# Optimization experiments

Hardware: AMD Instinct MI355X
Metric: run time of the kernel (lower is better)

The kernel has to match this reference:

```python
import jax, jax.numpy as jnp
import numpy as np

B, S, H, NH = 4, 1024, 1024, 16
DH = H // NH
EPS = 1e-12  # BERT layer_norm_eps


def layer_norm(x, scale, bias, eps=EPS):
    mu = jnp.mean(x, axis=-1, keepdims=True)
    var = jnp.var(x, axis=-1, keepdims=True)
    return (x - mu) / jnp.sqrt(var + eps) * scale + bias


def setup_inputs() -> dict:
    key = jax.random.key(0)
    ks = jax.random.split(key, 8)
    lin = lambda k: jax.random.normal(k, (H, H), jnp.float32) * 0.02
    zeros_h = jnp.zeros((H,), jnp.float32)
    return {
        "hidden_states": jax.random.normal(ks[0], (B, S, H), jnp.float32),
        "group_prob": jnp.zeros((B, S, S), jnp.float32),
        "attention_mask": jnp.ones((B, 1, S, S), jnp.int32),
        "Wq": lin(ks[1]), "bq": zeros_h,
        "Wk": lin(ks[2]), "bk": zeros_h,
        "Wv": lin(ks[3]), "bv": zeros_h,
        "gWq": lin(ks[4]), "gbq": zeros_h,
        "gWk": lin(ks[5]), "gbk": zeros_h,
        "g_ln_scale": jnp.ones((H,), jnp.float32), "g_ln_bias": zeros_h,
        "Wo": lin(ks[6]), "bo": zeros_h,
        "out_ln_scale": jnp.ones((H,), jnp.float32), "out_ln_bias": zeros_h,
    }


def _forward(hidden_states, group_prob, attention_mask, Wq, bq, Wk, bk, Wv, bv,
             gWq, gbq, gWk, gbk, g_ln_scale, g_ln_bias, Wo, bo,
             out_ln_scale, out_ln_bias):
    am = attention_mask.astype(jnp.int32)              # [B,1,S,S]
    a = jnp.eye(S, k=1, dtype=jnp.int32)               # superdiagonal
    b = jnp.eye(S, dtype=jnp.int32)                    # identity
    c = jnp.eye(S, k=-1, dtype=jnp.int32)              # subdiagonal
    tri = jnp.triu(jnp.ones((S, S), jnp.float32))      # upper tri incl diag

    # ---- GroupAttention (tree-transformer constituent priors) ----
    hs = layer_norm(hidden_states, g_ln_scale, g_ln_bias)
    gq = hs @ gWq.T + gbq
    gk = hs @ gWk.T + gbk
    g_scores = jnp.einsum('bqd,bkd->bqk', gq, gk) / jnp.float32(H)
    g_mask = (am & (a + c))[:, 0]                      # [B,S,S] tridiag band, no diag
    g_scores = jnp.where(g_mask == 0, -jnp.inf, g_scores)
    n_attn = jnp.nan_to_num(jax.nn.softmax(g_scores, axis=-1))
    n_attn = jnp.sqrt(n_attn * jnp.swapaxes(n_attn, -1, -2) + 1e-9)
    n_attn = group_prob + (1.0 - group_prob) * n_attn  # prior mixing
    t = jnp.where(a == 0, 0.0, jnp.log(n_attn + 1e-9)) @ tri
    g_attn = jnp.exp(tri @ t)
    strict_upper = tri.astype(jnp.int32) - b           # nonzero on strict upper tri
    g_attn = jnp.where(strict_upper == 0, 0.0, g_attn)
    g_attn = g_attn + jnp.swapaxes(g_attn, -1, -2) + jnp.where(b == 0, 1e-9, n_attn)
    break_prob = n_attn

    # ---- BertSelfAttention, mode 'L' ----
    def split_heads(x):
        return x.reshape(B, S, NH, DH).transpose(0, 2, 1, 3)  # [B,NH,S,DH]
    q = split_heads(hidden_states @ Wq.T + bq)
    k = split_heads(hidden_states @ Wk.T + bk)
    v = split_heads(hidden_states @ Wv.T + bv)
    scores = jnp.einsum('bhqd,bhkd->bhqk', q, k) / jnp.sqrt(jnp.float32(DH))
    keep = (am | b) != 0                               # diag always attended
    scores = jnp.where(keep, scores, -jnp.inf)
    probs = jax.nn.softmax(scores, axis=-1)
    probs = probs * g_attn[:, None]                    # group-prob reweighting
    ctx = jnp.einsum('bhqk,bhkd->bhqd', probs, v)
    ctx = ctx.transpose(0, 2, 1, 3).reshape(B, S, H)

    # ---- BertSelfOutput: dense + residual + LayerNorm ----
    out = layer_norm(ctx @ Wo.T + bo + hidden_states, out_ln_scale, out_ln_bias)
    return out, scores, g_attn, break_prob


def reference(hidden_states, group_prob, attention_mask, Wq, bq, Wk, bk, Wv, bv,
              gWq, gbq, gWk, gbk, g_ln_scale, g_ln_bias, Wo, bo,
              out_ln_scale, out_ln_bias):
    return _forward(hidden_states, group_prob, attention_mask, Wq, bq, Wk, bk,
                    Wv, bv, gWq, gbq, gWk, gbk, g_ln_scale, g_ln_bias, Wo, bo,
                    out_ln_scale, out_ln_bias)
```

## Files before the change

kernel.cpp:

```cpp
#include <hip/hip_runtime.h>
#include <math.h>

#define BB 4
#define S 1024
#define H 1024
#define NHD 16
#define DH 64
#define LN_EPS 1e-12f
#define SQ9 3.1622776601683795e-5f
#define NEG_INF (-__builtin_inff())
#define L2E 1.4426950408889634f

typedef unsigned short u16;
typedef unsigned int u32;
using bfrag = __attribute__((ext_vector_type(8))) short;
using f32x4 = __attribute__((ext_vector_type(4))) float;

typedef __attribute__((address_space(1))) void void_g;
typedef __attribute__((address_space(3))) void void_l;

__device__ __forceinline__ void gload16(const void* g, void* l) {
  __builtin_amdgcn_global_load_lds((void_g*)g, (void_l*)l, 16, 0, 0);
}

__device__ __forceinline__ u16 f2bf(float f) {
  u32 u = __builtin_bit_cast(u32, f);
  u32 r = (u + 0x7fffu + ((u >> 16) & 1u)) >> 16;
  return (u16)r;
}
__device__ __forceinline__ float bf2f(u32 b) {
  u32 u = b << 16;
  return __builtin_bit_cast(float, u);
}

__device__ __forceinline__ float sum16_dpp(float x) {
  int v;
  v = __builtin_amdgcn_mov_dpp(__builtin_bit_cast(int, x), 0xB1, 0xF, 0xF, true);
  x += __builtin_bit_cast(float, v);
  v = __builtin_amdgcn_mov_dpp(__builtin_bit_cast(int, x), 0x4E, 0xF, 0xF, true);
  x += __builtin_bit_cast(float, v);
  v = __builtin_amdgcn_mov_dpp(__builtin_bit_cast(int, x), 0x124, 0xF, 0xF, true);
  x += __builtin_bit_cast(float, v);
  v = __builtin_amdgcn_mov_dpp(__builtin_bit_cast(int, x), 0x128, 0xF, 0xF, true);
  x += __builtin_bit_cast(float, v);
  return x;
}

__device__ __forceinline__ float block_sum256(float v, float* buf) {
#pragma unroll
  for (int o = 32; o > 0; o >>= 1) v += __shfl_down(v, o);
  if ((threadIdx.x & 63) == 0) buf[threadIdx.x >> 6] = v;
  __syncthreads();
  float r = buf[0] + buf[1] + buf[2] + buf[3];
  __syncthreads();
  return r;
}

__global__ __launch_bounds__(256) void prep_kernel(
    const float* __restrict__ Wq, const float* __restrict__ Wk, const float* __restrict__ Wv,
    const float* __restrict__ gWq, const float* __restrict__ gWk,
    const float* __restrict__ hidden, const int* __restrict__ am,
    const float* __restrict__ glns, const float* __restrict__ glnb,
    u16* __restrict__ dstW, u32* __restrict__ amb, u16* __restrict__ hsbf) {
  __shared__ float buf[4];
  int bid = blockIdx.x;
  if (bid < 9216) {
    const int WQ = 262144;
    int i = bid * 256 + threadIdx.x;
    const float* src; int off;
    if      (i < 1 * WQ) { src = Wq;  off = 0; }
    else if (i < 2 * WQ) { src = Wk;  off = 1 * WQ; }
    else if (i < 3 * WQ) { src = Wv;  off = 2 * WQ; }
    else if (i < 4 * WQ) { src = gWq; off = 3 * WQ; }
    else if (i < 5 * WQ) { src = gWk; off = 4 * WQ; }
    else                 { src = hidden; off = 5 * WQ; }
    float4 v = reinterpret_cast<const float4*>(src)[i - off];
    u32 lo = (u32)f2bf(v.x) | ((u32)f2bf(v.y) << 16);
    u32 hi = (u32)f2bf(v.z) | ((u32)f2bf(v.w) << 16);
    reinterpret_cast<uint2*>(dstW)[i] = make_uint2(lo, hi);
  } else if (bid < 25600) {
    size_t t = (size_t)(bid - 9216) * 256 + threadIdx.x;
    int v = am[t] != 0;
    unsigned long long m = __ballot(v);
    int lane = threadIdx.x & 63;
    if (lane == 0)       amb[t >> 5] = (u32)m;
    else if (lane == 32) amb[t >> 5] = (u32)(m >> 32);
  } else {
    size_t row = bid - 25600;
    const float4 xv = reinterpret_cast<const float4*>(hidden + row * H)[threadIdx.x];
    float s  = xv.x + xv.y + xv.z + xv.w;
    float s2 = xv.x * xv.x + xv.y * xv.y + xv.z * xv.z + xv.w * xv.w;
    s  = block_sum256(s, buf);
    s2 = block_sum256(s2, buf);
    float mu  = s * (1.0f / H);
    float var = s2 * (1.0f / H) - mu * mu;
    float inv = rsqrtf(var + LN_EPS);
    const float4 sv = reinterpret_cast<const float4*>(glns)[threadIdx.x];
    const float4 bv = reinterpret_cast<const float4*>(glnb)[threadIdx.x];
    float o0 = (xv.x - mu) * inv * sv.x + bv.x;
    float o1 = (xv.y - mu) * inv * sv.y + bv.y;
    float o2 = (xv.z - mu) * inv * sv.z + bv.z;
    float o3 = (xv.w - mu) * inv * sv.w + bv.w;
    u32 lo = (u32)f2bf(o0) | ((u32)f2bf(o1) << 16);
    u32 hi = (u32)f2bf(o2) | ((u32)f2bf(o3) << 16);
    reinterpret_cast<uint2*>(hsbf + row * H)[threadIdx.x] = make_uint2(lo, hi);
  }
}

__global__ __launch_bounds__(256) void mega_gemm(
    const u16* __restrict__ hbf, const u16* __restrict__ hsbf,
    const u16* __restrict__ Wcat,
    const float* __restrict__ bq, const float* __restrict__ bk, const float* __restrict__ bv,
    const float* __restrict__ gbq, const float* __restrict__ gbk,
    u16* __restrict__ q, u16* __restrict__ k, u16* __restrict__ vt,
    u16* __restrict__ gq, u16* __restrict__ gk) {
  __shared__ __align__(16) u16 SM[32768];
  const int Kdim = H;
  int fid = blockIdx.x + blockIdx.y * 40;
  int swz = (fid & 7) * 160 + (fid >> 3);
  int lx = swz % 40, ly = swz / 40;
  int which = lx >> 3;
  const u16* A = (which < 3) ? hbf : hsbf;
  int rowBlk = ly * 128, colBlk = lx * 128;
  int tid = threadIdx.x, wid = tid >> 6, l = tid & 63;
  int dr = l >> 3, sl = l & 7;
  int co = (sl ^ dr) << 3;
  const u16* Ag = A + (size_t)rowBlk * Kdim;
  const u16* Bg = Wcat + (size_t)colBlk * Kdim;
  f32x4 acc[4][4];
#pragma unroll
  for (int i = 0; i < 4; ++i)
#pragma unroll
    for (int j = 0; j < 4; ++j) acc[i][j] = (f32x4){0.f, 0.f, 0.f, 0.f};
#pragma unroll
  for (int i = 0; i < 4; ++i) {
    int L = wid * 4 + i;
    gload16(Ag + (size_t)(L * 8 + dr) * Kdim + co, &SM[L * 512]);
    gload16(Bg + (size_t)(L * 8 + dr) * Kdim + co, &SM[16384 + L * 512]);
  }
  __syncthreads();
  int wm = wid >> 1, wn = wid & 1;
  const int nt = Kdim >> 6;
  int buf = 0;
  int sw = (l & 7) << 4;
  for (int t = 0; t < nt; ++t) {
    if (t + 1 < nt) {
      int k0 = (t + 1) << 6;
      int dstoff = (buf ^ 1) * 8192;
#pragma unroll
      for (int i = 0; i < 4; ++i) {
        int L = wid * 4 + i;
        gload16(Ag + (size_t)(L * 8 + dr) * Kdim + k0 + co, &SM[dstoff + L * 512]);
        gload16(Bg + (size_t)(L * 8 + dr) * Kdim + k0 + co, &SM[16384 + dstoff + L * 512]);
      }
    }
    const char* Ab = (const char*)&SM[buf * 8192];
    const char* Bb = (const char*)&SM[16384 + buf * 8192];
#pragma unroll
    for (int ks = 0; ks < 2; ++ks) {
      int kb = (ks * 64 + ((l >> 4) << 4)) ^ sw;
      bfrag af[4], bfv[4];
#pragma unroll
      for (int mi = 0; mi < 4; ++mi)
        af[mi] = *(const bfrag*)(Ab + (wm * 64 + mi * 16 + (l & 15)) * 128 + kb);
#pragma unroll
      for (int ni = 0; ni < 4; ++ni)
        bfv[ni] = *(const bfrag*)(Bb + (wn * 64 + ni * 16 + (l & 15)) * 128 + kb);
#pragma unroll
      for (int mi = 0; mi < 4; ++mi)
#pragma unroll
        for (int ni = 0; ni < 4; ++ni)
          acc[mi][ni] = __builtin_amdgcn_mfma_f32_16x16x32_bf16(af[mi], bfv[ni], acc[mi][ni], 0, 0, 0);
    }
    __syncthreads();
    buf ^= 1;
  }
  const float* bias = (which == 0) ? bq : (which == 1) ? bk : (which == 2) ? bv
                      : (which == 3) ? gbq : gbk;
  if (which == 2) {
    u16* T = SM;
#pragma unroll
    for (int mi = 0; mi < 4; ++mi) {
#pragma unroll
      for (int ni = 0; ni < 4; ++ni) {
        int c = wn * 64 + ni * 16 + (l & 15);
        float bvv = bias[(colBlk & 1023) + c];
        int tokb = wm * 64 + mi * 16 + ((l >> 4) << 2);
        u32 w0 = (u32)f2bf(acc[mi][ni][0] + bvv) | ((u32)f2bf(acc[mi][ni][1] + bvv) << 16);
        u32 w1 = (u32)f2bf(acc[mi][ni][2] + bvv) | ((u32)f2bf(acc[mi][ni][3] + bvv) << 16);
        *(u32*)&T[c * 144 + tokb]     = w0;
        *(u32*)&T[c * 144 + tokb + 2] = w1;
      }
    }
    __syncthreads();
    int col = tid >> 1, th = tid & 1;
    int g = (colBlk & 1023) + col;
    int bb = rowBlk >> 10;
    int s0 = (rowBlk & 1023) + th * 64;
    const uint4* src = (const uint4*)&T[col * 144 + th * 64];
    u16* dst = vt + ((size_t)(bb * 1024 + g)) * S + s0;
#pragma unroll
    for (int i = 0; i < 8; ++i) reinterpret_cast<uint4*>(dst)[i] = src[i];
  } else {
    u16* O = (which == 0) ? q : (which == 1) ? k : (which == 3) ? gq : gk;
#pragma unroll
    for (int mi = 0; mi < 4; ++mi) {
#pragma unroll
      for (int ni = 0; ni < 4; ++ni) {
        int col = (colBlk + wn * 64 + ni * 16 + (l & 15)) & 1023;
        float bvv = bias[col];
#pragma unroll
        for (int j = 0; j < 4; ++j) {
          int row = rowBlk + wm * 64 + mi * 16 + ((l >> 4) << 2) + j;
          O[(size_t)row * H + col] = f2bf(acc[mi][ni][j] + bvv);
        }
      }
    }
  }
}

__global__ __launch_bounds__(256) void gemm_dense(
    const u16* __restrict__ A, const u16* __restrict__ Bw,
    const float* __restrict__ bias, const float* __restrict__ resid,
    u16* __restrict__ C) {
  __shared__ __align__(16) u16 SM[32768];
  const int Kdim = H;
  int fid = blockIdx.x + blockIdx.y * 8;
  int swz = (fid & 7) * 32 + (fid >> 3);
  int lx = swz & 7, ly = swz >> 3;
  int rowBlk = ly * 128, colBlk = lx * 128;
  int tid = threadIdx.x, wid = tid >> 6, l = tid & 63;
  int dr = l >> 3, sl = l & 7;
  int co = (sl ^ dr) << 3;
  const u16* Ag = A + (size_t)rowBlk * Kdim;
  const u16* Bg = Bw + (size_t)colBlk * Kdim;
  f32x4 acc[4][4];
#pragma unroll
  for (int i = 0; i < 4; ++i)
#pragma unroll
    for (int j = 0; j < 4; ++j) acc[i][j] = (f32x4){0.f, 0.f, 0.f, 0.f};
#pragma unroll
  for (int i = 0; i < 4; ++i) {
    int L = wid * 4 + i;
    gload16(Ag + (size_t)(L * 8 + dr) * Kdim + co, &SM[L * 512]);
    gload16(Bg + (size_t)(L * 8 + dr) * Kdim + co, &SM[16384 + L * 512]);
  }
  __syncthreads();
  int wm = wid >> 1, wn = wid & 1;
  const int nt = Kdim >> 6;
  int buf = 0;
  int sw = (l & 7) << 4;
  for (int t = 0; t < nt; ++t) {
    if (t + 1 < nt) {
      int k0 = (t + 1) << 6;
      int dstoff = (buf ^ 1) * 8192;
#pragma unroll
      for (int i = 0; i < 4; ++i) {
        int L = wid * 4 + i;
        gload16(Ag + (size_t)(L * 8 + dr) * Kdim + k0 + co, &SM[dstoff + L * 512]);
        gload16(Bg + (size_t)(L * 8 + dr) * Kdim + k0 + co, &SM[16384 + dstoff + L * 512]);
      }
    }
    const char* Ab = (const char*)&SM[buf * 8192];
    const char* Bb = (const char*)&SM[16384 + buf * 8192];
#pragma unroll
    for (int ks = 0; ks < 2; ++ks) {
      int kb = (ks * 64 + ((l >> 4) << 4)) ^ sw;
      bfrag af[4], bfv[4];
#pragma unroll
      for (int mi = 0; mi < 4; ++mi)
        af[mi] = *(const bfrag*)(Ab + (wm * 64 + mi * 16 + (l & 15)) * 128 + kb);
#pragma unroll
      for (int ni = 0; ni < 4; ++ni)
        bfv[ni] = *(const bfrag*)(Bb + (wn * 64 + ni * 16 + (l & 15)) * 128 + kb);
#pragma unroll
      for (int mi = 0; mi < 4; ++mi)
#pragma unroll
        for (int ni = 0; ni < 4; ++ni)
          acc[mi][ni] = __builtin_amdgcn_mfma_f32_16x16x32_bf16(af[mi], bfv[ni], acc[mi][ni], 0, 0, 0);
    }
    __syncthreads();
    buf ^= 1;
  }
#pragma unroll
  for (int mi = 0; mi < 4; ++mi) {
#pragma unroll
    for (int ni = 0; ni < 4; ++ni) {
      int col = colBlk + wn * 64 + ni * 16 + (l & 15);
      float bvv = bias[col];
#pragma unroll
      for (int j = 0; j < 4; ++j) {
        int row = rowBlk + wm * 64 + mi * 16 + ((l >> 4) << 2) + j;
        C[(size_t)row * H + col] = f2bf(acc[mi][ni][j] + bvv + resid[(size_t)row * H + col]);
      }
    }
  }
}

__global__ __launch_bounds__(256) void band_dots_kernel(
    const u16* __restrict__ gq, const u16* __restrict__ gk,
    const float* __restrict__ Wo, u16* __restrict__ Wobf,
    float* __restrict__ znext, float* __restrict__ zprev) {
  __shared__ float buf[4];
  int bid = blockIdx.x;
  if (bid >= 4096) {
    int i = (bid - 4096) * 256 + threadIdx.x;
    float4 v = reinterpret_cast<const float4*>(Wo)[i];
    u32 lo = (u32)f2bf(v.x) | ((u32)f2bf(v.y) << 16);
    u32 hi = (u32)f2bf(v.z) | ((u32)f2bf(v.w) << 16);
    reinterpret_cast<uint2*>(Wobf)[i] = make_uint2(lo, hi);
    return;
  }
  size_t idx = bid;
  int i = (int)(idx & (S - 1));
  uint2 q2 = reinterpret_cast<const uint2*>(gq + idx * H)[threadIdx.x];
  float q0 = bf2f(q2.x & 0xffff), q1 = bf2f(q2.x >> 16);
  float q2f = bf2f(q2.y & 0xffff), q3 = bf2f(q2.y >> 16);
  float dn = 0.f, dp = 0.f;
  if (i < S - 1) {
    uint2 k2 = reinterpret_cast<const uint2*>(gk + (idx + 1) * H)[threadIdx.x];
    dn = q0 * bf2f(k2.x & 0xffff) + q1 * bf2f(k2.x >> 16) +
         q2f * bf2f(k2.y & 0xffff) + q3 * bf2f(k2.y >> 16);
  }
  if (i > 0) {
    uint2 k2 = reinterpret_cast<const uint2*>(gk + (idx - 1) * H)[threadIdx.x];
    dp = q0 * bf2f(k2.x & 0xffff) + q1 * bf2f(k2.x >> 16) +
         q2f * bf2f(k2.y & 0xffff) + q3 * bf2f(k2.y >> 16);
  }
  dn = block_sum256(dn, buf);
  dp = block_sum256(dp, buf);
  if (threadIdx.x == 0) { znext[idx] = dn; zprev[idx] = dp; }
}

__global__ __launch_bounds__(1024) void band_prefix_kernel(
    const float* __restrict__ znext, const float* __restrict__ zprev,
    const int* __restrict__ am, const float* __restrict__ gp,
    float* __restrict__ sband, float* __restrict__ Cpre) {
  __shared__ float pd[S];
  __shared__ float scn[S];
  int b = blockIdx.x, i = threadIdx.x;
  size_t idx = (size_t)b * S + i;
  bool luv = (i < S - 1) && (am[((size_t)b * S + i) * S + i + 1] != 0);
  bool ldv = (i > 0) && (am[((size_t)b * S + i) * S + i - 1] != 0);
  float pf, pdn;
  if (!luv && !ldv) { pf = 0.f; pdn = 0.f; }
  else if (!ldv)    { pf = 1.f; pdn = 0.f; }
  else if (!luv)    { pf = 0.f; pdn = 1.f; }
  else {
    float lu = znext[idx] * (1.0f / (float)H);
    float ld = zprev[idx] * (1.0f / (float)H);
    float m = fmaxf(lu, ld);
    float eu = expf(lu - m), ed = expf(ld - m);
    float inv = 1.f / (eu + ed);
    pf = eu * inv; pdn = ed * inv;
  }
  pd[i] = pdn;
  __syncthreads();
  float sb = 0.f, L = 0.f;
  if (i < S - 1) {
    sb = sqrtf(pf * pd[i + 1] + 1e-9f);
    float gpv = gp[((size_t)b * S + i) * S + (i + 1)];
    float nm = gpv + (1.f - gpv) * sb;
    L = logf(nm + 1e-9f);
  }
  sband[idx] = sb;
  scn[i] = L;
  __syncthreads();
  for (int off = 1; off < S; off <<= 1) {
    float t = (i >= off) ? scn[i - off] : 0.f;
    __syncthreads();
    scn[i] += t;
    __syncthreads();
  }
  Cpre[idx] = (i > 0) ? scn[i - 1] : 0.f;
}

__global__ __launch_bounds__(256) void gattn_write_kernel(
    const float* __restrict__ gp, const float* __restrict__ sband,
    const float* __restrict__ Cpre, float* __restrict__ ga, float* __restrict__ brk) {
  __shared__ float Crow[S];
  __shared__ float Srow[S];
  size_t bi = blockIdx.x;
  int b = (int)(bi >> 10), i = (int)(bi & (S - 1));
  reinterpret_cast<float4*>(Crow)[threadIdx.x] =
      reinterpret_cast<const float4*>(Cpre + (size_t)b * S)[threadIdx.x];
  reinterpret_cast<float4*>(Srow)[threadIdx.x] =
      reinterpret_cast<const float4*>(sband + (size_t)b * S)[threadIdx.x];
  __syncthreads();
  float Ci = Crow[i];
  size_t rowoff = bi * S;
  const float4 g4 = reinterpret_cast<const float4*>(gp + rowoff)[threadIdx.x];
  const float gparr[4] = {g4.x, g4.y, g4.z, g4.w};
  float go[4], bo_[4];
#pragma unroll
  for (int j = 0; j < 4; ++j) {
    int k = threadIdx.x * 4 + j;
    float gpv = gparr[j];
    float gav;
    if (k == i) {
      gav = gpv + (1.f - gpv) * SQ9;
    } else {
      float d = (k > i) ? (Crow[k] - Ci) : (Ci - Crow[k]);
      gav = expf(d) + 1e-9f;
    }
    float sval = (k == i + 1) ? Srow[i] : ((k == i - 1) ? Srow[k] : SQ9);
    go[j]  = gav;
    bo_[j] = gpv + (1.f - gpv) * sval;
  }
  f32x4 go4 = (f32x4){go[0], go[1], go[2], go[3]};
  __builtin_nontemporal_store(go4, reinterpret_cast<f32x4*>(ga + rowoff) + threadIdx.x);
  f32x4 bo4 = (f32x4){bo_[0], bo_[1], bo_[2], bo_[3]};
  __builtin_nontemporal_store(bo4, reinterpret_cast<f32x4*>(brk + rowoff) + threadIdx.x);
}

__global__ __launch_bounds__(512) void flash_kernel(
    const u16* __restrict__ q, const u16* __restrict__ k, const u16* __restrict__ vt,
    const u32* __restrict__ amb, const float* __restrict__ Cpre,
    const float* __restrict__ gp,
    float* __restrict__ scores, u16* __restrict__ ctx) {
  __shared__ __align__(16) u16 QPt[8192];
  __shared__ __align__(16) u16 Kt[2][4096];
  __shared__ __align__(16) u16 Vt[2][4096];
  __shared__ float CLds[1024];
  int fid = blockIdx.x + blockIdx.y * 8;
  int qb = (fid >> 3) & 7;
  int bh = (fid & 7) * 8 + (fid >> 6);
  int b = bh >> 4, h = bh & 15;
  int tid = threadIdx.x, wid = tid >> 6, l = tid & 63;
  int dr = l >> 3, sl = l & 7;
  int co = (sl ^ dr) << 3;
  const u16* qbase = q + ((size_t)b * S + qb * 128) * H + h * 64;
  const u16* kbase = k + (size_t)b * S * H + h * 64;
  const u16* vtb   = vt + (size_t)bh * 64 * S;
  {
    float2 c2 = reinterpret_cast<const float2*>(Cpre + (size_t)b * S)[tid];
    c2.x *= L2E; c2.y *= L2E;
    reinterpret_cast<float2*>(CLds)[tid] = c2;
  }
#pragma unroll
  for (int i = 0; i < 2; ++i) {
    int L = wid * 2 + i;
    gload16(qbase + (size_t)(L * 8 + dr) * H + co, &QPt[L * 512]);
  }
  gload16(kbase + (size_t)(wid * 8 + dr) * H + co, &Kt[0][wid * 512]);
  gload16(vtb + (size_t)(wid * 8 + dr) * S + co, &Vt[0][wid * 512]);
  __syncthreads();
  int sw = (l & 7) << 4;
  int qr = l & 15;
  bfrag qa[2];
#pragma unroll
  for (int ks = 0; ks < 2; ++ks) {
    int kb = (ks * 64 + ((l >> 4) << 4)) ^ sw;
    qa[ks] = *(const bfrag*)((const char*)QPt + (wid * 16 + qr) * 128 + kb);
  }
  __syncthreads();
  int rowg0 = qb * 128 + wid * 16 + ((l >> 4) << 2);
  float Ci2[4], gdiag[4];
#pragma unroll
  for (int j = 0; j < 4; ++j) {
    int row = rowg0 + j;
    Ci2[j] = CLds[row];
    float gpd = gp[((size_t)b * S + row) * S + row];
    gdiag[j] = gpd + (1.f - gpd) * SQ9;
  }
  float l_loc[4];
  f32x4 oacc[4];
#pragma unroll
  for (int j = 0; j < 4; ++j) l_loc[j] = 0.f;
#pragma unroll
  for (int nb = 0; nb < 4; ++nb) oacc[nb] = (f32x4){0.f, 0.f, 0.f, 0.f};
  uint2 wcur[4];
#pragma unroll
  for (int j = 0; j < 4; ++j)
    wcur[j] = *reinterpret_cast<const uint2*>(amb + ((size_t)b * S + rowg0 + j) * 32);
  int cur = 0;
  for (int kt = 0; kt < 16; ++kt) {
    uint2 wnxt[4];
    if (kt < 15) {
      gload16(kbase + (size_t)((kt + 1) * 64 + wid * 8 + dr) * H + co, &Kt[cur ^ 1][wid * 512]);
      gload16(vtb + (size_t)(wid * 8 + dr) * S + (kt + 1) * 64 + co, &Vt[cur ^ 1][wid * 512]);
#pragma unroll
      for (int j = 0; j < 4; ++j)
        wnxt[j] = *reinterpret_cast<const uint2*>(
            amb + ((size_t)b * S + rowg0 + j) * 32 + (kt + 1) * 2);
    }
    f32x4 acc[4];
#pragma unroll
    for (int nb = 0; nb < 4; ++nb) acc[nb] = (f32x4){0.f, 0.f, 0.f, 0.f};
    __builtin_amdgcn_s_setprio(1);
#pragma unroll
    for (int ks = 0; ks < 2; ++ks) {
      int kb = (ks * 64 + ((l >> 4) << 4)) ^ sw;
#pragma unroll
      for (int nb = 0; nb < 4; ++nb) {
        bfrag bv = *(const bfrag*)((const char*)Kt[cur] + (nb * 16 + qr) * 128 + kb);
        acc[nb] = __builtin_amdgcn_mfma_f32_16x16x32_bf16(qa[ks], bv, acc[nb], 0, 0, 0);
      }
    }
    __builtin_amdgcn_s_setprio(0);
    float vals[4][4];
#pragma unroll
    for (int j = 0; j < 4; ++j) {
      int row = rowg0 + j;
      float* srow = scores + ((size_t)bh * S + row) * S + kt * 64;
#pragma unroll
      for (int nb = 0; nb < 4; ++nb) {
        int col = nb * 16 + qr;
        int colg = kt * 64 + col;
        u32 word = (nb < 2) ? wcur[j].x : wcur[j].y;
        int keep = (int)((word >> (col & 31)) & 1u) | (row == colg);
        float v = keep ? acc[nb][j] * 0.125f : NEG_INF;
        vals[nb][j] = v;
        __builtin_nontemporal_store(v, srow + col);
      }
    }
    float Ck2[4];
#pragma unroll
    for (int nb = 0; nb < 4; ++nb) Ck2[nb] = CLds[kt * 64 + nb * 16 + qr];
#pragma unroll
    for (int j = 0; j < 4; ++j) {
      int row = rowg0 + j;
      int prow = wid * 16 + ((l >> 4) << 2) + j;
      char* ptrow = (char*)QPt + prow * 128;
      int psw = (prow & 7) << 4;
      float pp[4], pg[4];
#pragma unroll
      for (int nb = 0; nb < 4; ++nb) {
        float t = vals[nb][j] * L2E;
        pp[nb] = exp2f(t);
        int colg = kt * 64 + nb * 16 + qr;
        float d2 = (colg > row) ? (Ck2[nb] - Ci2[j]) : (Ci2[j] - Ck2[nb]);
        float g = exp2f(t + d2);
        pg[nb] = (colg == row) ? pp[nb] * gdiag[j] : g;
      }
      l_loc[j] += pp[0] + pp[1] + pp[2] + pp[3];
#pragma unroll
      for (int nb = 0; nb < 4; ++nb)
        *(u16*)(ptrow + (((nb * 16 + qr) * 2) ^ psw)) = f2bf(pg[nb]);
    }
    __builtin_amdgcn_s_setprio(1);
#pragma unroll
    for (int ks = 0; ks < 2; ++ks) {
      int kb = (ks * 64 + ((l >> 4) << 4)) ^ sw;
      bfrag pa = *(const bfrag*)((const char*)QPt + (wid * 16 + qr) * 128 + kb);
#pragma unroll
      for (int nb = 0; nb < 4; ++nb) {
        bfrag vv = *(const bfrag*)((const char*)Vt[cur] + (nb * 16 + qr) * 128 + kb);
        oacc[nb] = __builtin_amdgcn_mfma_f32_16x16x32_bf16(pa, vv, oacc[nb], 0, 0, 0);
      }
    }
    __builtin_amdgcn_s_setprio(0);
    asm volatile("s_waitcnt vmcnt(16)" ::: "memory");
    __builtin_amdgcn_s_barrier();
    __builtin_amdgcn_sched_barrier(0);
    if (kt < 15) {
#pragma unroll
      for (int j = 0; j < 4; ++j) wcur[j] = wnxt[j];
    }
    cur ^= 1;
  }
#pragma unroll
  for (int j = 0; j < 4; ++j) l_loc[j] = sum16_dpp(l_loc[j]);
#pragma unroll
  for (int j = 0; j < 4; ++j) {
    int row = rowg0 + j;
    float ir = 1.f / l_loc[j];
#pragma unroll
    for (int nb = 0; nb < 4; ++nb) {
      int d = nb * 16 + qr;
      ctx[((size_t)b * S + row) * H + h * 64 + d] = f2bf(oacc[nb][j] * ir);
    }
  }
}

__global__ __launch_bounds__(256) void ln_bf_kernel(
    const u16* __restrict__ x, const float* __restrict__ sc,
    const float* __restrict__ bi, float* __restrict__ y) {
  __shared__ float buf[4];
  size_t row = blockIdx.x;
  uint2 xv = reinterpret_cast<const uint2*>(x + row * H)[threadIdx.x];
  float x0 = bf2f(xv.x & 0xffff), x1 = bf2f(xv.x >> 16);
  float x2 = bf2f(xv.y & 0xffff), x3 = bf2f(xv.y >> 16);
  float s  = x0 + x1 + x2 + x3;
  float s2 = x0 * x0 + x1 * x1 + x2 * x2 + x3 * x3;
  s  = block_sum256(s, buf);
  s2 = block_sum256(s2, buf);
  float mu  = s * (1.0f / H);
  float var = s2 * (1.0f / H) - mu * mu;
  float inv = rsqrtf(var + LN_EPS);
  const float4 sv = reinterpret_cast<const float4*>(sc)[threadIdx.x];
  const float4 bv = reinterpret_cast<const float4*>(bi)[threadIdx.x];
  float4 o;
  o.x = (x0 - mu) * inv * sv.x + bv.x;
  o.y = (x1 - mu) * inv * sv.y + bv.y;
  o.z = (x2 - mu) * inv * sv.z + bv.z;
  o.w = (x3 - mu) * inv * sv.w + bv.w;
  reinterpret_cast<float4*>(y + row * H)[threadIdx.x] = o;
}

extern "C" void kernel_launch(void* const* d_in, const int* in_sizes, int n_in,
                              void* d_out, int out_size, void* d_ws, size_t ws_size,
                              hipStream_t stream) {
  const float* hidden = (const float*)d_in[0];
  const float* gp     = (const float*)d_in[1];
  const int*   am     = (const int*)d_in[2];
  const float* Wq = (const float*)d_in[3];  const float* bq = (const float*)d_in[4];
  const float* Wk = (const float*)d_in[5];  const float* bk = (const float*)d_in[6];
  const float* Wv = (const float*)d_in[7];  const float* bv = (const float*)d_in[8];
  const float* gWq = (const float*)d_in[9]; const float* gbq = (const float*)d_in[10];
  const float* gWk = (const float*)d_in[11];const float* gbk = (const float*)d_in[12];
  const float* glns = (const float*)d_in[13]; const float* glnb = (const float*)d_in[14];
  const float* Wo = (const float*)d_in[15]; const float* bo = (const float*)d_in[16];
  const float* olns = (const float*)d_in[17]; const float* olnb = (const float*)d_in[18];

  float* out    = (float*)d_out;
  float* scores = out + (size_t)BB * S * H;
  float* gattn  = scores + (size_t)BB * NHD * S * S;
  float* brk    = gattn + (size_t)BB * S * S;

  const size_t MB = 1u << 20;
  char* w = (char*)d_ws;
  u16* Wcat  = (u16*)(w);
  u16* hbf   = (u16*)(w + 10 * MB);
  u16* ctxbf = hbf;
  u16* hsbf  = (u16*)(w + 18 * MB);
  u16* Wobf  = hsbf;
  u16* qbf   = (u16*)(w + 26 * MB);
  u16* kbf   = (u16*)(w + 34 * MB);
  u16* vtb   = (u16*)(w + 42 * MB);
  u16* gqbf  = (u16*)(w + 50 * MB);
  u16* densebf = gqbf;
  u16* gkbf  = (u16*)(w + 58 * MB);
  u32* amb   = (u32*)(w + 66 * MB);
  float* znext  = (float*)(w + 66 * MB + 512 * 1024);
  float* zprev  = znext + BB * S;
  float* sbandA = zprev + BB * S;
  float* CpreA  = sbandA + BB * S;

  dim3 blk(256);

  prep_kernel<<<29696, blk, 0, stream>>>(Wq, Wk, Wv, gWq, gWk, hidden, am,
                                         glns, glnb, Wcat, amb, hsbf);

  mega_gemm<<<dim3(40, 32), blk, 0, stream>>>(hbf, hsbf, Wcat,
                                              bq, bk, bv, gbq, gbk,
                                              qbf, kbf, vtb, gqbf, gkbf);

  band_dots_kernel<<<5120, blk, 0, stream>>>(gqbf, gkbf, Wo, Wobf, znext, zprev);
  band_prefix_kernel<<<BB, 1024, 0, stream>>>(znext, zprev, am, gp, sbandA, CpreA);
  gattn_write_kernel<<<BB * S, blk, 0, stream>>>(gp, sbandA, CpreA, gattn, brk);

  flash_kernel<<<dim3(8, 64), dim3(512), 0, stream>>>(qbf, kbf, vtb, amb, CpreA,
                                                      gp, scores, ctxbf);

  gemm_dense<<<dim3(8, 32), blk, 0, stream>>>(ctxbf, Wobf, bo, hidden, densebf);
  ln_bf_kernel<<<BB * S, blk, 0, stream>>>(densebf, olns, olnb, out);
}
```

Before: 230.1 us.

## Transpose QK^T MFMA so each lane owns a row, vectorize score and P stores

Swaps the MFMA operand order for S = QK^T so the accumulator holds a transposed tile, giving each lane one query row and four consecutive key columns. This lets the scores output be written as 16-byte nontemporal vector stores instead of scalar stores, lets the bf16 P tile be written to LDS as packed 64-bit stores, and reduces per-lane mask and diagonal state to a single row. The row-sum for normalization now needs a cross-lane shuffle plus an LDS exchange and barrier, because the output accumulator layout still maps rows differently from the score layout.

```diff
diff --git a/kernel.cpp b/kernel.cpp
--- a/kernel.cpp
+++ b/kernel.cpp
@@ -13,6 +13,7 @@
 
 typedef unsigned short u16;
 typedef unsigned int u32;
+typedef unsigned long long u64;
 using bfrag = __attribute__((ext_vector_type(8))) short;
 using f32x4 = __attribute__((ext_vector_type(4))) float;
 
@@ -31,19 +32,6 @@
 __device__ __forceinline__ float bf2f(u32 b) {
   u32 u = b << 16;
   return __builtin_bit_cast(float, u);
-}
-
-__device__ __forceinline__ float sum16_dpp(float x) {
-  int v;
-  v = __builtin_amdgcn_mov_dpp(__builtin_bit_cast(int, x), 0xB1, 0xF, 0xF, true);
-  x += __builtin_bit_cast(float, v);
-  v = __builtin_amdgcn_mov_dpp(__builtin_bit_cast(int, x), 0x4E, 0xF, 0xF, true);
-  x += __builtin_bit_cast(float, v);
-  v = __builtin_amdgcn_mov_dpp(__builtin_bit_cast(int, x), 0x124, 0xF, 0xF, true);
-  x += __builtin_bit_cast(float, v);
-  v = __builtin_amdgcn_mov_dpp(__builtin_bit_cast(int, x), 0x128, 0xF, 0xF, true);
-  x += __builtin_bit_cast(float, v);
-  return x;
 }
 
 __device__ __forceinline__ float block_sum256(float v, float* buf) {
@@ -422,11 +410,13 @@
   __shared__ __align__(16) u16 Kt[2][4096];
   __shared__ __align__(16) u16 Vt[2][4096];
   __shared__ float CLds[1024];
+  __shared__ float Lsc[128];
   int fid = blockIdx.x + blockIdx.y * 8;
   int qb = (fid >> 3) & 7;
   int bh = (fid & 7) * 8 + (fid >> 6);
   int b = bh >> 4, h = bh & 15;
   int tid = threadIdx.x, wid = tid >> 6, l = tid & 63;
+  int hi = l >> 4, qr = l & 15;
   int dr = l >> 3, sl = l & 7;
   int co = (sl ^ dr) << 3;
   const u16* qbase = q + ((size_t)b * S + qb * 128) * H + h * 64;
@@ -446,43 +436,33 @@
   gload16(vtb + (size_t)(wid * 8 + dr) * S + co, &Vt[0][wid * 512]);
   __syncthreads();
   int sw = (l & 7) << 4;
-  int qr = l & 15;
   bfrag qa[2];
 #pragma unroll
   for (int ks = 0; ks < 2; ++ks) {
-    int kb = (ks * 64 + ((l >> 4) << 4)) ^ sw;
+    int kb = (ks * 64 + (hi << 4)) ^ sw;
     qa[ks] = *(const bfrag*)((const char*)QPt + (wid * 16 + qr) * 128 + kb);
   }
   __syncthreads();
-  int rowg0 = qb * 128 + wid * 16 + ((l >> 4) << 2);
-  float Ci2[4], gdiag[4];
-#pragma unroll
-  for (int j = 0; j < 4; ++j) {
-    int row = rowg0 + j;
-    Ci2[j] = CLds[row];
-    float gpd = gp[((size_t)b * S + row) * S + row];
-    gdiag[j] = gpd + (1.f - gpd) * SQ9;
-  }
-  float l_loc[4];
+  int myrow = qb * 128 + wid * 16 + qr;
+  float Ci2 = CLds[myrow];
+  float gpd = gp[((size_t)b * S + myrow) * S + myrow];
+  float gdiagS = gpd + (1.f - gpd) * SQ9;
+  float* srowbase = scores + ((size_t)bh * S + myrow) * S;
+  char* ptrow = (char*)QPt + (wid * 16 + qr) * 128;
+  int psw = (qr & 7) << 4;
+  float l_loc = 0.f;
   f32x4 oacc[4];
 #pragma unroll
-  for (int j = 0; j < 4; ++j) l_loc[j] = 0.f;
-#pragma unroll
   for (int nb = 0; nb < 4; ++nb) oacc[nb] = (f32x4){0.f, 0.f, 0.f, 0.f};
-  uint2 wcur[4];
-#pragma unroll
-  for (int j = 0; j < 4; ++j)
-    wcur[j] = *reinterpret_cast<const uint2*>(amb + ((size_t)b * S + rowg0 + j) * 32);
+  uint2 wcur = *reinterpret_cast<const uint2*>(amb + (size_t)myrow * 32 + (size_t)b * S * 32);
   int cur = 0;
   for (int kt = 0; kt < 16; ++kt) {
-    uint2 wnxt[4];
+    uint2 wnxt;
     if (kt < 15) {
       gload16(kbase + (size_t)((kt + 1) * 64 + wid * 8 + dr) * H + co, &Kt[cur ^ 1][wid * 512]);
       gload16(vtb + (size_t)(wid * 8 + dr) * S + (kt + 1) * 64 + co, &Vt[cur ^ 1][wid * 512]);
-#pragma unroll
-      for (int j = 0; j < 4; ++j)
-        wnxt[j] = *reinterpret_cast<const uint2*>(
-            amb + ((size_t)b * S + rowg0 + j) * 32 + (kt + 1) * 2);
+      wnxt = *reinterpret_cast<const uint2*>(
+          amb + ((size_t)b * S + myrow) * 32 + (kt + 1) * 2);
     }
     f32x4 acc[4];
 #pragma unroll
@@ -490,58 +470,45 @@
     __builtin_amdgcn_s_setprio(1);
 #pragma unroll
     for (int ks = 0; ks < 2; ++ks) {
-      int kb = (ks * 64 + ((l >> 4) << 4)) ^ sw;
+      int kb = (ks * 64 + (hi << 4)) ^ sw;
 #pragma unroll
       for (int nb = 0; nb < 4; ++nb) {
-        bfrag bv = *(const bfrag*)((const char*)Kt[cur] + (nb * 16 + qr) * 128 + kb);
-        acc[nb] = __builtin_amdgcn_mfma_f32_16x16x32_bf16(qa[ks], bv, acc[nb], 0, 0, 0);
+        bfrag kf = *(const bfrag*)((const char*)Kt[cur] + (nb * 16 + qr) * 128 + kb);
+        acc[nb] = __builtin_amdgcn_mfma_f32_16x16x32_bf16(kf, qa[ks], acc[nb], 0, 0, 0);
       }
     }
     __builtin_amdgcn_s_setprio(0);
-    float vals[4][4];
-#pragma unroll
-    for (int j = 0; j < 4; ++j) {
-      int row = rowg0 + j;
-      float* srow = scores + ((size_t)bh * S + row) * S + kt * 64;
-#pragma unroll
-      for (int nb = 0; nb < 4; ++nb) {
-        int col = nb * 16 + qr;
-        int colg = kt * 64 + col;
-        u32 word = (nb < 2) ? wcur[j].x : wcur[j].y;
-        int keep = (int)((word >> (col & 31)) & 1u) | (row == colg);
+#pragma unroll
+    for (int nb = 0; nb < 4; ++nb) {
+      int kloc0 = nb * 16 + hi * 4;
+      int bit0 = (nb & 1) * 16 + hi * 4;
+      u32 word = (nb < 2) ? wcur.x : wcur.y;
+      f32x4 sv;
+      float pp[4], pg[4];
+      const float4 ck4 = *reinterpret_cast<const float4*>(&CLds[kt * 64 + kloc0]);
+      const float ck[4] = {ck4.x, ck4.y, ck4.z, ck4.w};
+#pragma unroll
+      for (int j = 0; j < 4; ++j) {
+        int colg = kt * 64 + kloc0 + j;
+        int keep = (int)((word >> (bit0 + j)) & 1u) | (colg == myrow);
         float v = keep ? acc[nb][j] * 0.125f : NEG_INF;
-        vals[nb][j] = v;
-        __builtin_nontemporal_store(v, srow + col);
-      }
-    }
-    float Ck2[4];
-#pragma unroll
-    for (int nb = 0; nb < 4; ++nb) Ck2[nb] = CLds[kt * 64 + nb * 16 + qr];
-#pragma unroll
-    for (int j = 0; j < 4; ++j) {
-      int row = rowg0 + j;
-      int prow = wid * 16 + ((l >> 4) << 2) + j;
-      char* ptrow = (char*)QPt + prow * 128;
-      int psw = (prow & 7) << 4;
-      float pp[4], pg[4];
-#pragma unroll
-      for (int nb = 0; nb < 4; ++nb) {
-        float t = vals[nb][j] * L2E;
-        pp[nb] = exp2f(t);
-        int colg = kt * 64 + nb * 16 + qr;
-        float d2 = (colg > row) ? (Ck2[nb] - Ci2[j]) : (Ci2[j] - Ck2[nb]);
+        sv[j] = v;
+        float t = v * L2E;
+        pp[j] = exp2f(t);
+        float d2 = (colg > myrow) ? (ck[j] - Ci2) : (Ci2 - ck[j]);
         float g = exp2f(t + d2);
-        pg[nb] = (colg == row) ? pp[nb] * gdiag[j] : g;
-      }
-      l_loc[j] += pp[0] + pp[1] + pp[2] + pp[3];
-#pragma unroll
-      for (int nb = 0; nb < 4; ++nb)
-        *(u16*)(ptrow + (((nb * 16 + qr) * 2) ^ psw)) = f2bf(pg[nb]);
+        pg[j] = (colg == myrow) ? pp[j] * gdiagS : g;
+      }
+      __builtin_nontemporal_store(sv, reinterpret_cast<f32x4*>(srowbase + kt * 64 + kloc0));
+      l_loc += pp[0] + pp[1] + pp[2] + pp[3];
+      u64 pk = (u64)f2bf(pg[0]) | ((u64)f2bf(pg[1]) << 16) |
+               ((u64)f2bf(pg[2]) << 32) | ((u64)f2bf(pg[3]) << 48);
+      *(u64*)(ptrow + ((nb * 32 + hi * 8) ^ psw)) = pk;
     }
     __builtin_amdgcn_s_setprio(1);
 #pragma unroll
     for (int ks = 0; ks < 2; ++ks) {
-      int kb = (ks * 64 + ((l >> 4) << 4)) ^ sw;
+      int kb = (ks * 64 + (hi << 4)) ^ sw;
       bfrag pa = *(const bfrag*)((const char*)QPt + (wid * 16 + qr) * 128 + kb);
 #pragma unroll
       for (int nb = 0; nb < 4; ++nb) {
@@ -553,22 +520,23 @@
     asm volatile("s_waitcnt vmcnt(16)" ::: "memory");
     __builtin_amdgcn_s_barrier();
     __builtin_amdgcn_sched_barrier(0);
-    if (kt < 15) {
-#pragma unroll
-      for (int j = 0; j < 4; ++j) wcur[j] = wnxt[j];
-    }
+    if (kt < 15) wcur = wnxt;
     cur ^= 1;
   }
-#pragma unroll
-  for (int j = 0; j < 4; ++j) l_loc[j] = sum16_dpp(l_loc[j]);
+  l_loc += __shfl_xor(l_loc, 16);
+  l_loc += __shfl_xor(l_loc, 32);
+  if (hi == 0) Lsc[wid * 16 + qr] = l_loc;
+  __builtin_amdgcn_s_barrier();
+  float ir[4];
+#pragma unroll
+  for (int j = 0; j < 4; ++j) ir[j] = 1.f / Lsc[wid * 16 + hi * 4 + j];
 #pragma unroll
   for (int j = 0; j < 4; ++j) {
-    int row = rowg0 + j;
-    float ir = 1.f / l_loc[j];
+    int row = qb * 128 + wid * 16 + hi * 4 + j;
 #pragma unroll
     for (int nb = 0; nb < 4; ++nb) {
       int d = nb * 16 + qr;
-      ctx[((size_t)b * S + row) * H + h * 64 + d] = f2bf(oacc[nb][j] * ir);
+      ctx[((size_t)b * S + row) * H + h * 64 + d] = f2bf(oacc[nb][j] * ir[j]);
     }
   }
 }
```

Result: slower. 240.2 us (+4.4%).
